# Optimization experiments

Measured on AMD Instinct MI355X. Metric: run time of the kernel, lower is better.

The kernel has to match this reference:

```python
import jax, jax.numpy as jnp
import numpy as np

B, D, H, W, C = 2, 28, 28, 28, 96
HEADS = 3
WS = (7, 7, 7)
SS = (3, 3, 3)
N = WS[0] * WS[1] * WS[2]  # 343 tokens per window
MLP_DIM = 4 * C


def _rel_pos_index():
    coords = np.stack(np.meshgrid(np.arange(WS[0]), np.arange(WS[1]), np.arange(WS[2]), indexing='ij'))
    cf = coords.reshape(3, -1)
    rel = (cf[:, :, None] - cf[:, None, :]).transpose(1, 2, 0)
    rel[..., 0] += WS[0] - 1
    rel[..., 1] += WS[1] - 1
    rel[..., 2] += WS[2] - 1
    rel[..., 0] *= (2 * WS[1] - 1) * (2 * WS[2] - 1)
    rel[..., 1] *= 2 * WS[2] - 1
    return rel.sum(-1)  # [N, N] int


def _compute_mask():
    # shifted-window attention mask (MONAI compute_mask)
    img = np.zeros((1, D, H, W, 1), np.float32)
    cnt = 0.0
    for ds in (slice(0, -WS[0]), slice(-WS[0], -SS[0]), slice(-SS[0], None)):
        for hs in (slice(0, -WS[1]), slice(-WS[1], -SS[1]), slice(-SS[1], None)):
            for ws_ in (slice(0, -WS[2]), slice(-WS[2], -SS[2]), slice(-SS[2], None)):
                img[:, ds, hs, ws_, :] = cnt
                cnt += 1.0
    mw = img.reshape(1, D // WS[0], WS[0], H // WS[1], WS[1], W // WS[2], WS[2], 1)
    mw = mw.transpose(0, 1, 3, 5, 2, 4, 6, 7).reshape(-1, N)  # [nw, N]
    diff = mw[:, None, :] - mw[:, :, None]
    return np.where(diff != 0, -100.0, 0.0).astype(np.float32)  # [nw, N, N]


def _ln(x, g, b):
    mu = x.mean(-1, keepdims=True)
    var = ((x - mu) ** 2).mean(-1, keepdims=True)
    return (x - mu) * jax.lax.rsqrt(var + 1e-5) * g + b


def setup_inputs() -> dict:
    key = jax.random.key(0)
    ks = jax.random.split(key, 8)
    f = lambda k, shape: (jax.random.normal(k, shape) * 0.02).astype(jnp.float32)
    n_bias = (2 * WS[0] - 1) * (2 * WS[1] - 1) * (2 * WS[2] - 1)
    return {
        'x': jax.random.normal(ks[0], (B, D, H, W, C), jnp.float32),
        'mask_matrix': jnp.asarray(_compute_mask()),
        'g1': jnp.ones((C,), jnp.float32), 'b1': jnp.zeros((C,), jnp.float32),
        'w_qkv': f(ks[1], (3 * C, C)), 'b_qkv': jnp.zeros((3 * C,), jnp.float32),
        'bias_table': f(ks[2], (n_bias, HEADS)),
        'w_proj': f(ks[3], (C, C)), 'b_proj': jnp.zeros((C,), jnp.float32),
        'g2': jnp.ones((C,), jnp.float32), 'b2': jnp.zeros((C,), jnp.float32),
        'w_fc1': f(ks[4], (MLP_DIM, C)), 'b_fc1': jnp.zeros((MLP_DIM,), jnp.float32),
        'w_fc2': f(ks[5], (C, MLP_DIM)), 'b_fc2': jnp.zeros((C,), jnp.float32),
        'rel_index': jnp.asarray(_rel_pos_index(), dtype=jnp.int32),
    }


def reference(x, mask_matrix, g1, b1, w_qkv, b_qkv, bias_table, w_proj, b_proj,
              g2, b2, w_fc1, b_fc1, w_fc2, b_fc2, rel_index):
    shortcut = x
    h = _ln(x, g1, b1)
    # cyclic shift
    h = jnp.roll(h, (-SS[0], -SS[1], -SS[2]), axis=(1, 2, 3))
    # window partition -> [B_, N, C]
    win = h.reshape(B, D // WS[0], WS[0], H // WS[1], WS[1], W // WS[2], WS[2], C)
    win = win.transpose(0, 1, 3, 5, 2, 4, 6, 7).reshape(-1, N, C)
    Bw = win.shape[0]
    hd = C // HEADS
    qkv = (win @ w_qkv.T + b_qkv).reshape(Bw, N, 3, HEADS, hd).transpose(2, 0, 3, 1, 4)
    q, k, v = qkv[0] * (hd ** -0.5), qkv[1], qkv[2]
    attn = jnp.einsum('bhnd,bhmd->bhnm', q, k)  # [Bw, H, N, N]
    bias = bias_table[rel_index.reshape(-1)].reshape(N, N, HEADS).transpose(2, 0, 1)
    attn = attn + bias[None]
    nw = mask_matrix.shape[0]
    attn = attn.reshape(Bw // nw, nw, HEADS, N, N) + mask_matrix[None, :, None]
    attn = jax.nn.softmax(attn.reshape(Bw, HEADS, N, N), axis=-1)
    out = jnp.einsum('bhnm,bhmd->bhnd', attn, v).transpose(0, 2, 1, 3).reshape(Bw, N, C)
    out = out @ w_proj.T + b_proj
    # window reverse -> [B, D, H, W, C]
    out = out.reshape(B, D // WS[0], H // WS[1], W // WS[2], WS[0], WS[1], WS[2], C)
    out = out.transpose(0, 1, 4, 2, 5, 3, 6, 7).reshape(B, D, H, W, C)
    # reverse cyclic shift
    out = jnp.roll(out, SS, axis=(1, 2, 3))
    x = shortcut + out
    h2 = _ln(x, g2, b2)
    h2 = jax.nn.gelu(h2 @ w_fc1.T + b_fc1, approximate=False)
    return x + (h2 @ w_fc2.T + b_fc2)
```

## Files before the change

kernel.cpp:

```cpp
#include <hip/hip_runtime.h>
#include <hip/hip_bf16.h>
#include <math.h>

typedef unsigned short u16;
typedef unsigned int u32;
typedef unsigned char u8;

#define T_TOK 43904
#define NTOK 343
#define LOG2E 1.4426950408889634f
#define MASKV 144.26950408889634f

typedef __attribute__((ext_vector_type(4))) float f32x4;
typedef __attribute__((ext_vector_type(8))) short s16x8;

__device__ __forceinline__ float bf2f(u32 v) { return __uint_as_float(v << 16); }
__device__ __forceinline__ u16 f2bf(float f) {
  u32 u = __float_as_uint(f);
  return (u16)((u + 0x7fffu + ((u >> 16) & 1u)) >> 16);
}

__device__ __forceinline__ float ldf(const void* p, int f32, size_t i) {
  return f32 ? ((const float*)p)[i] : bf2f(((const u16*)p)[i]);
}
__device__ __forceinline__ float2 ld2(const void* p, int f32, size_t i) {
  if (f32) return *(const float2*)((const float*)p + i);
  u32 pk = *(const u32*)((const u16*)p + i);
  return make_float2(bf2f(pk & 0xffff), bf2f(pk >> 16));
}

__device__ __forceinline__ size_t spatial_base(int t) {
  int win = t / 343, n = t - win * 343;
  int bb = win >> 6, wrem = win & 63;
  int wd = wrem >> 4, wh = (wrem >> 2) & 3, ww = wrem & 3;
  int td = n / 49; int r = n - td * 49; int th = r / 7; int tw = r - th * 7;
  int d0 = wd * 7 + td + 3; if (d0 >= 28) d0 -= 28;
  int h0 = wh * 7 + th + 3; if (h0 >= 28) h0 -= 28;
  int w0 = ww * 7 + tw + 3; if (w0 >= 28) w0 -= 28;
  return (size_t)(((bb * 28 + d0) * 28 + h0) * 28 + w0) * 96;
}

__device__ __forceinline__ int zone3(int p) { return p < 21 ? 0 : (p < 25 ? 1 : 2); }
__device__ __forceinline__ int cid_of(int mw, int n) {
  int td = n / 49, rr = n - td * 49, th = rr / 7, tw = rr - th * 7;
  int d = (mw >> 4) * 7 + td, h = ((mw >> 2) & 3) * 7 + th, w = (mw & 3) * 7 + tw;
  return zone3(d) * 9 + zone3(h) * 3 + zone3(w);
}

__global__ __launch_bounds__(64) void detect_kernel(const u16* __restrict__ x, int* __restrict__ flag) {
  int lane = threadIdx.x;
  int bad = 0;
  #pragma unroll
  for (int q = 0; q < 8; q++) {
    u16 b = x[(lane * 8 + q) * 2];
    int e = (b >> 7) & 0xff;
    if (e >= 0x90) bad = 1;
  }
  unsigned long long m = __ballot(bad);
  if (lane == 0) *flag = (m != 0ull) ? 1 : 0;
}

__global__ __launch_bounds__(256) void wconv_kernel(
    const void* __restrict__ w0, const void* __restrict__ w1,
    const void* __restrict__ w2, const void* __restrict__ w3,
    u16* __restrict__ out, const int* __restrict__ dflag) {
  int f32 = __builtin_amdgcn_readfirstlane(dflag[0]);
  int g = blockIdx.x * 256 + threadIdx.x;
  if (g >= 110592) return;
  float v;
  if (g < 27648)      v = ldf(w0, f32, g);
  else if (g < 36864) v = ldf(w1, f32, g - 27648);
  else if (g < 73728) v = ldf(w2, f32, g - 36864);
  else                v = ldf(w3, f32, g - 73728);
  out[g] = f2bf(v);
}

__global__ __launch_bounds__(256) void ln_gather_kernel(
    const void* __restrict__ x, const void* __restrict__ g, const void* __restrict__ b,
    u16* __restrict__ outw, const int* __restrict__ dflag) {
  int f32 = __builtin_amdgcn_readfirstlane(dflag[0]);
  int t = blockIdx.x * 4 + (threadIdx.x >> 6);
  int lane = threadIdx.x & 63;
  size_t base = spatial_base(t);
  int c = lane * 2;
  float vx = 0.f, vy = 0.f;
  if (c < 96) { float2 p = ld2(x, f32, base + c); vx = p.x; vy = p.y; }
  float s = vx + vy, ss = vx * vx + vy * vy;
  #pragma unroll
  for (int o = 1; o < 64; o <<= 1) { s += __shfl_xor(s, o); ss += __shfl_xor(ss, o); }
  float mean = s * (1.f / 96.f);
  float var = ss * (1.f / 96.f) - mean * mean;
  float rstd = rsqrtf(var + 1e-5f);
  if (c < 96) {
    float2 gp = ld2(g, f32, c), bp = ld2(b, f32, c);
    float y0 = (vx - mean) * rstd * gp.x + bp.x;
    float y1 = (vy - mean) * rstd * gp.y + bp.y;
    *(u32*)(outw + (size_t)t * 96 + c) = (u32)f2bf(y0) | ((u32)f2bf(y1) << 16);
  }
}

__global__ __launch_bounds__(256) void b3m_kernel(
    const void* __restrict__ bias_table, const int* __restrict__ rel,
    u16* __restrict__ b3m, const int* __restrict__ dflag) {
  int f32 = __builtin_amdgcn_readfirstlane(dflag[0]);
  int row = blockIdx.x;
  int by = blockIdx.y;
  int cls = by / 3, head = by - cls * 3;
  int mw = ((cls & 4) ? 48 : 0) | ((cls & 2) ? 12 : 0) | ((cls & 1) ? 3 : 0);
  int cidq = cid_of(mw, row);
  for (int col = threadIdx.x; col < 352; col += 256) {
    float v = -MASKV;
    if (col < 343) {
      v = ldf(bias_table, f32, (size_t)rel[row * 343 + col] * 3 + head) * LOG2E;
      if (cid_of(mw, col) != cidq) v -= MASKV;
    }
    b3m[((size_t)by * 343 + row) * 352 + col] = f2bf(v);
  }
}

__global__ __launch_bounds__(256) void qkv_kernel(
    const u16* __restrict__ A, const u16* __restrict__ Wb, const void* __restrict__ bias,
    u16* __restrict__ outp, const int* __restrict__ dflag) {
  int f32 = __builtin_amdgcn_readfirstlane(dflag[0]);
  __shared__ alignas(16) u16 As[128 * 104];
  __shared__ alignas(16) u16 Ws[96 * 104];
  int tid = threadIdx.x;
  int m0 = blockIdx.x * 128, n0 = blockIdx.y * 96;
  int w = tid >> 6, lane = tid & 63, quad = lane >> 4, l16 = lane & 15;
  f32x4 acc[2][6];
  #pragma unroll
  for (int i = 0; i < 2; i++)
    #pragma unroll
    for (int j = 0; j < 6; j++) acc[i][j] = (f32x4){0.f, 0.f, 0.f, 0.f};
  for (int i = tid; i < 1536; i += 256) {
    int row = i / 12; int c = (i - row * 12) * 8;
    *(uint4*)&As[row * 104 + c] = *(const uint4*)(A + (size_t)(m0 + row) * 96 + c);
  }
  for (int i = tid; i < 1152; i += 256) {
    int row = i / 12; int c = (i - row * 12) * 8;
    *(uint4*)&Ws[row * 104 + c] = *(const uint4*)(Wb + (size_t)(n0 + row) * 96 + c);
  }
  __syncthreads();
  #pragma unroll
  for (int kc = 0; kc < 3; kc++) {
    s16x8 fa0 = *(const s16x8*)&As[(w * 32 + l16) * 104 + kc * 32 + quad * 8];
    s16x8 fa1 = *(const s16x8*)&As[(w * 32 + 16 + l16) * 104 + kc * 32 + quad * 8];
    #pragma unroll
    for (int j = 0; j < 6; j++) {
      s16x8 fb = *(const s16x8*)&Ws[(j * 16 + l16) * 104 + kc * 32 + quad * 8];
      acc[0][j] = __builtin_amdgcn_mfma_f32_16x16x32_bf16(fa0, fb, acc[0][j], 0, 0, 0);
      acc[1][j] = __builtin_amdgcn_mfma_f32_16x16x32_bf16(fa1, fb, acc[1][j], 0, 0, 0);
    }
  }
  #pragma unroll
  for (int i = 0; i < 2; i++) {
    #pragma unroll
    for (int r = 0; r < 4; r++) {
      int mm = m0 + w * 32 + i * 16 + quad * 4 + r;
      #pragma unroll
      for (int j = 0; j < 6; j++) {
        int nn = n0 + j * 16 + l16;
        float v = acc[i][j][r] + ldf(bias, f32, nn);
        int sel = nn / 96, hd = (nn - sel * 96) >> 5, cc = nn & 31;
        float scl = (sel == 0) ? 0.25504208f : 1.0f;
        outp[((size_t)(sel * 3 + hd) * T_TOK + mm) * 32 + cc] = f2bf(v * scl);
      }
    }
  }
}

__device__ __forceinline__ int vsw(int ch) { return ((ch >> 1) ^ (ch >> 3)) & 3; }

__global__ __launch_bounds__(512) void attn_mfma_kernel(
    const u16* __restrict__ qkv, const u16* __restrict__ b3m,
    u16* __restrict__ attnb) {
  __shared__ alignas(16) u16 Ks[352 * 32];
  __shared__ alignas(16) u16 Vt[32 * 352];
  __shared__ alignas(16) u16 Ps[8][512];

  int tid = threadIdx.x;
  int wh = blockIdx.y;
  int head = wh % 3;
  int win = wh / 3;
  int mw = win & 63;
  int cls = (((mw >> 4) == 3) ? 4 : 0) | ((((mw >> 2) & 3) == 3) ? 2 : 0) | (((mw & 3) == 3) ? 1 : 0);
  int m0 = blockIdx.x * 128;
  size_t wbase = (size_t)win * NTOK;

  const u16* qplane = qkv + ((size_t)head * T_TOK + wbase) * 32;
  const u16* kplane = qkv + ((size_t)(3 + head) * T_TOK + wbase) * 32;
  const u16* vplane = qkv + ((size_t)(6 + head) * T_TOK + wbase) * 32;

  for (int i = tid; i < 1408; i += 512) {
    int tok = i >> 2, cb = i & 3;
    uint4 kv = make_uint4(0, 0, 0, 0);
    if (tok < 343) kv = *(const uint4*)(kplane + (size_t)tok * 32 + cb * 8);
    *(uint4*)&Ks[tok * 32 + 8 * (cb ^ (tok & 3))] = kv;
  }
  for (int i = tid; i < 688; i += 512) {
    int p = i >> 2, cb = (i & 3) * 8;
    int t0 = 2 * p;
    uint4 v0 = *(const uint4*)(vplane + (size_t)t0 * 32 + cb);
    uint4 v1 = make_uint4(0, 0, 0, 0);
    if (t0 + 1 < 343) v1 = *(const uint4*)(vplane + (size_t)(t0 + 1) * 32 + cb);
    u32 a0[4] = {v0.x, v0.y, v0.z, v0.w};
    u32 a1[4] = {v1.x, v1.y, v1.z, v1.w};
    int blk = t0 >> 3, tin = (t0 & 7) >> 1;
    #pragma unroll
    for (int q = 0; q < 4; q++) {
      int ch0 = cb + 2 * q;
      u32 w0v = (a0[q] & 0xffffu) | ((a1[q] & 0xffffu) << 16);
      u32 w1v = (a0[q] >> 16) | (a1[q] & 0xffff0000u);
      ((u32*)Vt)[ch0 * 176 + 4 * (blk ^ vsw(ch0)) + tin] = w0v;
      ((u32*)Vt)[(ch0 + 1) * 176 + 4 * (blk ^ vsw(ch0 + 1)) + tin] = w1v;
    }
  }
  if (tid < 256) {
    int ch = tid >> 3, j = tid & 7;
    Vt[ch * 352 + 8 * (43 ^ vsw(ch)) + j] = 0;
  }
  __syncthreads();

  int w = tid >> 6, lane = tid & 63, quad = lane >> 4, l16 = lane & 15;
  int qbase = m0 + w * 16;
  int qrow_l = qbase + l16;
  int qc = qrow_l < NTOK ? qrow_l : NTOK - 1;
  s16x8 fq = *(const s16x8*)(qplane + (size_t)qc * 32 + quad * 8);
  const u16* bmrow = b3m + ((size_t)(cls * 3 + head) * 343 + qc) * 352;
  int swl = (l16 ^ (l16 >> 2)) & 3;
  int vsw0 = vsw(l16), vsw1 = vsw(16 + l16);

  float lsum = 0.f;
  f32x4 o0 = {0.f, 0.f, 0.f, 0.f}, o1 = {0.f, 0.f, 0.f, 0.f};
  const f32x4 zz = {0.f, 0.f, 0.f, 0.f};

  for (int t32 = 0; t32 < 11; t32++) {
    #pragma unroll
    for (int h = 0; h < 2; h++) {
      int kb = t32 * 32 + h * 16;
      int ktok = kb + l16;
      s16x8 fk = *(const s16x8*)&Ks[ktok * 32 + 8 * (quad ^ (ktok & 3))];
      f32x4 st = __builtin_amdgcn_mfma_f32_16x16x32_bf16(fk, fq, zz, 0, 0, 0);
      uint2 bm = *(const uint2*)(bmrow + kb + quad * 4);
      float p0 = exp2f(st[0] + bf2f(bm.x & 0xffff));
      float p1 = exp2f(st[1] + bf2f(bm.x >> 16));
      float p2 = exp2f(st[2] + bf2f(bm.y & 0xffff));
      float p3 = exp2f(st[3] + bf2f(bm.y >> 16));
      lsum += (p0 + p1) + (p2 + p3);
      u32 pa = (__float_as_uint(p0) >> 16) | (__float_as_uint(p1) & 0xffff0000u);
      u32 pb = (__float_as_uint(p2) >> 16) | (__float_as_uint(p3) & 0xffff0000u);
      int blkp = h * 2 + (quad >> 1);
      *(uint2*)&Ps[w][l16 * 32 + 8 * (blkp ^ swl) + (quad & 1) * 4] = make_uint2(pa, pb);
    }
    s16x8 fp  = *(const s16x8*)&Ps[w][l16 * 32 + 8 * (quad ^ swl)];
    s16x8 fv0 = *(const s16x8*)&Vt[l16 * 352 + 8 * ((t32 * 4 + quad) ^ vsw0)];
    s16x8 fv1 = *(const s16x8*)&Vt[(16 + l16) * 352 + 8 * ((t32 * 4 + quad) ^ vsw1)];
    o0 = __builtin_amdgcn_mfma_f32_16x16x32_bf16(fp, fv0, o0, 0, 0, 0);
    o1 = __builtin_amdgcn_mfma_f32_16x16x32_bf16(fp, fv1, o1, 0, 0, 0);
  }

  lsum += __shfl_xor(lsum, 16);
  lsum += __shfl_xor(lsum, 32);
  #pragma unroll
  for (int r = 0; r < 4; r++) {
    int qrow = qbase + quad * 4 + r;
    float ls = __shfl(lsum, quad * 4 + r);
    if (qrow < NTOK) {
      float rs = 1.0f / ls;
      size_t ob = (wbase + qrow) * 96 + head * 32;
      attnb[ob + l16] = f2bf(o0[r] * rs);
      attnb[ob + 16 + l16] = f2bf(o1[r] * rs);
    }
  }
}

__global__ __launch_bounds__(256) void mlp_fused_kernel(
    const u16* __restrict__ attnb, const u16* __restrict__ wcat,
    const void* __restrict__ x, const void* __restrict__ b_proj,
    const void* __restrict__ g2, const void* __restrict__ b2,
    const void* __restrict__ b_fc1, const void* __restrict__ b_fc2,
    void* __restrict__ outp, const int* __restrict__ dflag) {
  int f32 = __builtin_amdgcn_readfirstlane(dflag[0]);
  __shared__ alignas(16) u16 As[64 * 104];
  __shared__ alignas(16) u16 As2[64 * 104];
  __shared__ alignas(16) u16 Ws[96 * 104];
  const u16* w_projb = wcat + 27648;
  const u16* w_fc1b  = wcat + 36864;
  const u16* w_fc2b  = wcat + 73728;
  int tid = threadIdx.x, m0 = blockIdx.x * 64;
  int w = tid >> 6, lane = tid & 63, quad = lane >> 4, l16 = lane & 15;

  for (int i = tid; i < 768; i += 256) {
    int row = i / 12, c = (i - row * 12) * 8;
    *(uint4*)&As[row * 104 + c] = *(const uint4*)(attnb + (size_t)(m0 + row) * 96 + c);
  }
  for (int i = tid; i < 1152; i += 256) {
    int row = i / 12, c = (i - row * 12) * 8;
    *(uint4*)&Ws[row * 104 + c] = *(const uint4*)(w_projb + row * 96 + c);
  }
  __syncthreads();
  f32x4 accp[6];
  #pragma unroll
  for (int j = 0; j < 6; j++) accp[j] = (f32x4){0.f, 0.f, 0.f, 0.f};
  #pragma unroll
  for (int kc = 0; kc < 3; kc++) {
    s16x8 fa = *(const s16x8*)&As[(w * 16 + l16) * 104 + kc * 32 + quad * 8];
    #pragma unroll
    for (int j = 0; j < 6; j++) {
      s16x8 fb = *(const s16x8*)&Ws[(j * 16 + l16) * 104 + kc * 32 + quad * 8];
      accp[j] = __builtin_amdgcn_mfma_f32_16x16x32_bf16(fa, fb, accp[j], 0, 0, 0);
    }
  }
  __syncthreads();

  float bp[6], gv[6], b2v[6];
  #pragma unroll
  for (int j = 0; j < 6; j++) {
    int nn = j * 16 + l16;
    bp[j] = ldf(b_proj, f32, nn); gv[j] = ldf(g2, f32, nn); b2v[j] = ldf(b2, f32, nn);
  }
  float rv[4][6];
  size_t sb[4];
  #pragma unroll
  for (int r = 0; r < 4; r++) {
    int mm = m0 + w * 16 + quad * 4 + r;
    sb[r] = spatial_base(mm);
    float s = 0.f, ss = 0.f;
    #pragma unroll
    for (int j = 0; j < 6; j++) {
      float v = accp[j][r] + bp[j] + ldf(x, f32, sb[r] + j * 16 + l16);
      rv[r][j] = v; s += v; ss += v * v;
    }
    #pragma unroll
    for (int o = 1; o < 16; o <<= 1) { s += __shfl_xor(s, o); ss += __shfl_xor(ss, o); }
    float mean = s * (1.f / 96.f);
    float var = ss * (1.f / 96.f) - mean * mean;
    float rstd = rsqrtf(var + 1e-5f);
    #pragma unroll
    for (int j = 0; j < 6; j++)
      As[(w * 16 + quad * 4 + r) * 104 + j * 16 + l16] = f2bf((rv[r][j] - mean) * rstd * gv[j] + b2v[j]);
  }

  f32x4 acc2[6];
  #pragma unroll
  for (int j = 0; j < 6; j++) acc2[j] = (f32x4){0.f, 0.f, 0.f, 0.f};
  for (int c = 0; c < 4; c++) {
    __syncthreads();
    for (int i = tid; i < 1152; i += 256) {
      int row = i / 12, cc = (i - row * 12) * 8;
      *(uint4*)&Ws[row * 104 + cc] = *(const uint4*)(w_fc1b + (size_t)(96 * c + row) * 96 + cc);
    }
    __syncthreads();
    f32x4 a1[6];
    #pragma unroll
    for (int j = 0; j < 6; j++) a1[j] = (f32x4){0.f, 0.f, 0.f, 0.f};
    #pragma unroll
    for (int kc = 0; kc < 3; kc++) {
      s16x8 fa = *(const s16x8*)&As[(w * 16 + l16) * 104 + kc * 32 + quad * 8];
      #pragma unroll
      for (int j = 0; j < 6; j++) {
        s16x8 fb = *(const s16x8*)&Ws[(j * 16 + l16) * 104 + kc * 32 + quad * 8];
        a1[j] = __builtin_amdgcn_mfma_f32_16x16x32_bf16(fa, fb, a1[j], 0, 0, 0);
      }
    }
    #pragma unroll
    for (int j = 0; j < 6; j++) {
      float bf1 = ldf(b_fc1, f32, 96 * c + j * 16 + l16);
      #pragma unroll
      for (int r = 0; r < 4; r++) {
        float v = a1[j][r] + bf1;
        v = 0.5f * v * (1.0f + erff(v * 0.70710678118f));
        As2[(w * 16 + quad * 4 + r) * 104 + j * 16 + l16] = f2bf(v);
      }
    }
    __syncthreads();
    for (int i = tid; i < 1152; i += 256) {
      int row = i / 12, cc = (i - row * 12) * 8;
      *(uint4*)&Ws[row * 104 + cc] = *(const uint4*)(w_fc2b + (size_t)row * 384 + 96 * c + cc);
    }
    __syncthreads();
    #pragma unroll
    for (int kc = 0; kc < 3; kc++) {
      s16x8 fa2 = *(const s16x8*)&As2[(w * 16 + l16) * 104 + kc * 32 + quad * 8];
      #pragma unroll
      for (int j = 0; j < 6; j++) {
        s16x8 fb = *(const s16x8*)&Ws[(j * 16 + l16) * 104 + kc * 32 + quad * 8];
        acc2[j] = __builtin_amdgcn_mfma_f32_16x16x32_bf16(fa2, fb, acc2[j], 0, 0, 0);
      }
    }
  }
  float bf2v[6];
  #pragma unroll
  for (int j = 0; j < 6; j++) bf2v[j] = ldf(b_fc2, f32, j * 16 + l16);
  #pragma unroll
  for (int r = 0; r < 4; r++) {
    #pragma unroll
    for (int j = 0; j < 6; j++) {
      float v = acc2[j][r] + bf2v[j] + rv[r][j];
      if (f32) ((float*)outp)[sb[r] + j * 16 + l16] = v;
      else     ((u16*)outp)[sb[r] + j * 16 + l16] = f2bf(v);
    }
  }
}

extern "C" void kernel_launch(void* const* d_in, const int* in_sizes, int n_in,
                              void* d_out, int out_size, void* d_ws, size_t ws_size,
                              hipStream_t stream) {
  (void)in_sizes; (void)n_in; (void)out_size; (void)ws_size;
  const void* x       = d_in[0];
  const void* g1      = d_in[2];
  const void* b1      = d_in[3];
  const void* w_qkv   = d_in[4];
  const void* b_qkv   = d_in[5];
  const void* bias_tb = d_in[6];
  const void* w_proj  = d_in[7];
  const void* b_proj  = d_in[8];
  const void* g2      = d_in[9];
  const void* b2      = d_in[10];
  const void* w_fc1   = d_in[11];
  const void* b_fc1   = d_in[12];
  const void* w_fc2   = d_in[13];
  const void* b_fc2   = d_in[14];
  const int* rel_idx  = (const int*)d_in[15];

  char* ws = (char*)d_ws;
  int*  dflag = (int*)ws;
  u16*  winb  = (u16*)(ws + 256);
  u16*  qkvb  = (u16*)(ws + 8429824);
  u16*  attnb = (u16*)(ws + 33718528);
  u16*  b3mb  = (u16*)(ws + 42148096);
  u16*  wcat  = (u16*)(ws + 47943424);
  u16*  w_qkvb = wcat;

  detect_kernel<<<1, 64, 0, stream>>>((const u16*)x, dflag);
  wconv_kernel<<<432, 256, 0, stream>>>(w_qkv, w_proj, w_fc1, w_fc2, wcat, dflag);
  b3m_kernel<<<dim3(343, 24), 256, 0, stream>>>(bias_tb, rel_idx, b3mb, dflag);
  ln_gather_kernel<<<T_TOK / 4, 256, 0, stream>>>(x, g1, b1, winb, dflag);
  qkv_kernel<<<dim3(343, 3), 256, 0, stream>>>(winb, w_qkvb, b_qkv, qkvb, dflag);
  attn_mfma_kernel<<<dim3(3, 384), 512, 0, stream>>>(qkvb, b3mb, attnb);
  mlp_fused_kernel<<<686, 256, 0, stream>>>(attnb, wcat, x, b_proj, g2, b2,
                                            b_fc1, b_fc2, d_out, dflag);
}
```

Before: 228.7 us.

## Fuse LN into QKV GEMM, merge setup kernels, prefetch MLP weights

```diff
diff --git a/kernel.cpp b/kernel.cpp
--- a/kernel.cpp
+++ b/kernel.cpp
@@ -23,10 +23,29 @@
 __device__ __forceinline__ float ldf(const void* p, int f32, size_t i) {
   return f32 ? ((const float*)p)[i] : bf2f(((const u16*)p)[i]);
 }
-__device__ __forceinline__ float2 ld2(const void* p, int f32, size_t i) {
-  if (f32) return *(const float2*)((const float*)p + i);
-  u32 pk = *(const u32*)((const u16*)p + i);
-  return make_float2(bf2f(pk & 0xffff), bf2f(pk >> 16));
+__device__ __forceinline__ void ld8(const void* p, int f32, size_t i, float* o) {
+  if (f32) {
+    float4 a = *(const float4*)((const float*)p + i);
+    float4 b = *(const float4*)((const float*)p + i + 4);
+    o[0] = a.x; o[1] = a.y; o[2] = a.z; o[3] = a.w;
+    o[4] = b.x; o[5] = b.y; o[6] = b.z; o[7] = b.w;
+  } else {
+    uint4 pk = *(const uint4*)((const u16*)p + i);
+    u32 v[4] = {pk.x, pk.y, pk.z, pk.w};
+    #pragma unroll
+    for (int q = 0; q < 4; q++) { o[2 * q] = bf2f(v[q] & 0xffff); o[2 * q + 1] = bf2f(v[q] >> 16); }
+  }
+}
+
+__device__ __forceinline__ int detect_f32x(const u16* xr) {
+  int lane = threadIdx.x & 63;
+  int bad = 0;
+  #pragma unroll
+  for (int q = 0; q < 8; q++) {
+    u16 b = xr[(lane * 8 + q) * 2];
+    if (((b >> 7) & 0xff) >= 0x90) bad = 1;
+  }
+  return (__ballot(bad) != 0ull) ? 1 : 0;
 }
 
 __device__ __forceinline__ size_t spatial_base(int t) {
@@ -47,100 +66,104 @@
   return zone3(d) * 9 + zone3(h) * 3 + zone3(w);
 }
 
-__global__ __launch_bounds__(64) void detect_kernel(const u16* __restrict__ x, int* __restrict__ flag) {
-  int lane = threadIdx.x;
-  int bad = 0;
-  #pragma unroll
-  for (int q = 0; q < 8; q++) {
-    u16 b = x[(lane * 8 + q) * 2];
-    int e = (b >> 7) & 0xff;
-    if (e >= 0x90) bad = 1;
-  }
-  unsigned long long m = __ballot(bad);
-  if (lane == 0) *flag = (m != 0ull) ? 1 : 0;
-}
-
-__global__ __launch_bounds__(256) void wconv_kernel(
+__global__ __launch_bounds__(256) void setup_kernel(
+    const u16* __restrict__ x,
     const void* __restrict__ w0, const void* __restrict__ w1,
     const void* __restrict__ w2, const void* __restrict__ w3,
-    u16* __restrict__ out, const int* __restrict__ dflag) {
-  int f32 = __builtin_amdgcn_readfirstlane(dflag[0]);
-  int g = blockIdx.x * 256 + threadIdx.x;
-  if (g >= 110592) return;
-  float v;
-  if (g < 27648)      v = ldf(w0, f32, g);
-  else if (g < 36864) v = ldf(w1, f32, g - 27648);
-  else if (g < 73728) v = ldf(w2, f32, g - 36864);
-  else                v = ldf(w3, f32, g - 73728);
-  out[g] = f2bf(v);
-}
-
-__global__ __launch_bounds__(256) void ln_gather_kernel(
-    const void* __restrict__ x, const void* __restrict__ g, const void* __restrict__ b,
-    u16* __restrict__ outw, const int* __restrict__ dflag) {
-  int f32 = __builtin_amdgcn_readfirstlane(dflag[0]);
-  int t = blockIdx.x * 4 + (threadIdx.x >> 6);
-  int lane = threadIdx.x & 63;
-  size_t base = spatial_base(t);
-  int c = lane * 2;
-  float vx = 0.f, vy = 0.f;
-  if (c < 96) { float2 p = ld2(x, f32, base + c); vx = p.x; vy = p.y; }
-  float s = vx + vy, ss = vx * vx + vy * vy;
-  #pragma unroll
-  for (int o = 1; o < 64; o <<= 1) { s += __shfl_xor(s, o); ss += __shfl_xor(ss, o); }
-  float mean = s * (1.f / 96.f);
-  float var = ss * (1.f / 96.f) - mean * mean;
-  float rstd = rsqrtf(var + 1e-5f);
-  if (c < 96) {
-    float2 gp = ld2(g, f32, c), bp = ld2(b, f32, c);
-    float y0 = (vx - mean) * rstd * gp.x + bp.x;
-    float y1 = (vy - mean) * rstd * gp.y + bp.y;
-    *(u32*)(outw + (size_t)t * 96 + c) = (u32)f2bf(y0) | ((u32)f2bf(y1) << 16);
-  }
-}
-
-__global__ __launch_bounds__(256) void b3m_kernel(
     const void* __restrict__ bias_table, const int* __restrict__ rel,
-    u16* __restrict__ b3m, const int* __restrict__ dflag) {
-  int f32 = __builtin_amdgcn_readfirstlane(dflag[0]);
-  int row = blockIdx.x;
-  int by = blockIdx.y;
-  int cls = by / 3, head = by - cls * 3;
-  int mw = ((cls & 4) ? 48 : 0) | ((cls & 2) ? 12 : 0) | ((cls & 1) ? 3 : 0);
-  int cidq = cid_of(mw, row);
-  for (int col = threadIdx.x; col < 352; col += 256) {
-    float v = -MASKV;
-    if (col < 343) {
-      v = ldf(bias_table, f32, (size_t)rel[row * 343 + col] * 3 + head) * LOG2E;
-      if (cid_of(mw, col) != cidq) v -= MASKV;
-    }
-    b3m[((size_t)by * 343 + row) * 352 + col] = f2bf(v);
-  }
-}
-
-__global__ __launch_bounds__(256) void qkv_kernel(
-    const u16* __restrict__ A, const u16* __restrict__ Wb, const void* __restrict__ bias,
-    u16* __restrict__ outp, const int* __restrict__ dflag) {
-  int f32 = __builtin_amdgcn_readfirstlane(dflag[0]);
+    u16* __restrict__ wcat, u16* __restrict__ b3m) {
+  int f32 = detect_f32x(x);
+  int b = blockIdx.x;
+  if (b < 432) {
+    int g = b * 256 + threadIdx.x;
+    if (g < 110592) {
+      float v;
+      if (g < 27648)      v = ldf(w0, f32, g);
+      else if (g < 36864) v = ldf(w1, f32, g - 27648);
+      else if (g < 73728) v = ldf(w2, f32, g - 36864);
+      else                v = ldf(w3, f32, g - 73728);
+      wcat[g] = f2bf(v);
+    }
+    return;
+  }
+  int row = b - 432;
+  for (int by = 0; by < 24; by++) {
+    int cls = by / 3, head = by - cls * 3;
+    int mw = ((cls & 4) ? 48 : 0) | ((cls & 2) ? 12 : 0) | ((cls & 1) ? 3 : 0);
+    int cidq = cid_of(mw, row);
+    for (int col = threadIdx.x; col < 352; col += 256) {
+      float v = -MASKV;
+      if (col < 343) {
+        v = ldf(bias_table, f32, (size_t)rel[row * 343 + col] * 3 + head) * LOG2E;
+        if (cid_of(mw, col) != cidq) v -= MASKV;
+      }
+      b3m[((size_t)by * 343 + row) * 352 + col] = f2bf(v);
+    }
+  }
+}
+
+__global__ __launch_bounds__(256) void qkv_ln_kernel(
+    const void* __restrict__ x, const void* __restrict__ g1, const void* __restrict__ b1,
+    const u16* __restrict__ Wb, const void* __restrict__ bias,
+    u16* __restrict__ outp) {
+  int f32 = detect_f32x((const u16*)x);
   __shared__ alignas(16) u16 As[128 * 104];
   __shared__ alignas(16) u16 Ws[96 * 104];
+  __shared__ float gld[96], bld[96];
   int tid = threadIdx.x;
   int m0 = blockIdx.x * 128, n0 = blockIdx.y * 96;
   int w = tid >> 6, lane = tid & 63, quad = lane >> 4, l16 = lane & 15;
+
+  for (int i = tid; i < 1536; i += 256) {
+    int row = i / 12, cc = (i - row * 12) * 8;
+    size_t sb = spatial_base(m0 + row);
+    float f[8];
+    ld8(x, f32, sb + cc, f);
+    uint4 pk;
+    pk.x = (u32)f2bf(f[0]) | ((u32)f2bf(f[1]) << 16);
+    pk.y = (u32)f2bf(f[2]) | ((u32)f2bf(f[3]) << 16);
+    pk.z = (u32)f2bf(f[4]) | ((u32)f2bf(f[5]) << 16);
+    pk.w = (u32)f2bf(f[6]) | ((u32)f2bf(f[7]) << 16);
+    *(uint4*)&As[row * 104 + cc] = pk;
+  }
+  for (int i = tid; i < 1152; i += 256) {
+    int row = i / 12, cc = (i - row * 12) * 8;
+    *(uint4*)&Ws[row * 104 + cc] = *(const uint4*)(Wb + (size_t)(n0 + row) * 96 + cc);
+  }
+  if (tid < 96) { gld[tid] = ldf(g1, f32, tid); bld[tid] = ldf(b1, f32, tid); }
+  __syncthreads();
+
+  {
+    int row = tid >> 1, half = tid & 1;
+    u32* rp = (u32*)&As[row * 104] + half * 24;
+    float s = 0.f, ss = 0.f;
+    #pragma unroll
+    for (int m = 0; m < 24; m++) {
+      u32 pk = rp[m];
+      float a = bf2f(pk & 0xffff), b = bf2f(pk >> 16);
+      s += a + b; ss += a * a + b * b;
+    }
+    s += __shfl_xor(s, 1); ss += __shfl_xor(ss, 1);
+    float mean = s * (1.f / 96.f);
+    float var = ss * (1.f / 96.f) - mean * mean;
+    float rstd = rsqrtf(var + 1e-5f);
+    int cbase = half * 48;
+    #pragma unroll
+    for (int m = 0; m < 24; m++) {
+      u32 pk = rp[m];
+      float a = bf2f(pk & 0xffff), b = bf2f(pk >> 16);
+      a = (a - mean) * rstd * gld[cbase + 2 * m] + bld[cbase + 2 * m];
+      b = (b - mean) * rstd * gld[cbase + 2 * m + 1] + bld[cbase + 2 * m + 1];
+      rp[m] = (u32)f2bf(a) | ((u32)f2bf(b) << 16);
+    }
+  }
+  __syncthreads();
+
   f32x4 acc[2][6];
   #pragma unroll
   for (int i = 0; i < 2; i++)
     #pragma unroll
     for (int j = 0; j < 6; j++) acc[i][j] = (f32x4){0.f, 0.f, 0.f, 0.f};
-  for (int i = tid; i < 1536; i += 256) {
-    int row = i / 12; int c = (i - row * 12) * 8;
-    *(uint4*)&As[row * 104 + c] = *(const uint4*)(A + (size_t)(m0 + row) * 96 + c);
-  }
-  for (int i = tid; i < 1152; i += 256) {
-    int row = i / 12; int c = (i - row * 12) * 8;
-    *(uint4*)&Ws[row * 104 + c] = *(const uint4*)(Wb + (size_t)(n0 + row) * 96 + c);
-  }
-  __syncthreads();
   #pragma unroll
   for (int kc = 0; kc < 3; kc++) {
     s16x8 fa0 = *(const s16x8*)&As[(w * 32 + l16) * 104 + kc * 32 + quad * 8];
@@ -274,13 +297,35 @@
   }
 }
 
+struct PF { uint4 v[5]; };
+__device__ __forceinline__ void pf_load(PF& p, const u16* base, int rowstride, int coloff, int tid) {
+  #pragma unroll
+  for (int t = 0; t < 5; t++) {
+    int idx = tid + t * 256;
+    if (idx < 1152) {
+      int row = idx / 12, cc = (idx - row * 12) * 8;
+      p.v[t] = *(const uint4*)(base + (size_t)row * rowstride + coloff + cc);
+    }
+  }
+}
+__device__ __forceinline__ void pf_commit(const PF& p, u16* Ws, int tid) {
+  #pragma unroll
+  for (int t = 0; t < 5; t++) {
+    int idx = tid + t * 256;
+    if (idx < 1152) {
+      int row = idx / 12, cc = (idx - row * 12) * 8;
+      *(uint4*)&Ws[row * 104 + cc] = p.v[t];
+    }
+  }
+}
+
 __global__ __launch_bounds__(256) void mlp_fused_kernel(
     const u16* __restrict__ attnb, const u16* __restrict__ wcat,
     const void* __restrict__ x, const void* __restrict__ b_proj,
     const void* __restrict__ g2, const void* __restrict__ b2,
     const void* __restrict__ b_fc1, const void* __restrict__ b_fc2,
-    void* __restrict__ outp, const int* __restrict__ dflag) {
-  int f32 = __builtin_amdgcn_readfirstlane(dflag[0]);
+    void* __restrict__ outp) {
+  int f32 = detect_f32x((const u16*)x);
   __shared__ alignas(16) u16 As[64 * 104];
   __shared__ alignas(16) u16 As2[64 * 104];
   __shared__ alignas(16) u16 Ws[96 * 104];
@@ -290,15 +335,17 @@
   int tid = threadIdx.x, m0 = blockIdx.x * 64;
   int w = tid >> 6, lane = tid & 63, quad = lane >> 4, l16 = lane & 15;
 
+  PF p;
+  pf_load(p, w_projb, 96, 0, tid);
   for (int i = tid; i < 768; i += 256) {
     int row = i / 12, c = (i - row * 12) * 8;
     *(uint4*)&As[row * 104 + c] = *(const uint4*)(attnb + (size_t)(m0 + row) * 96 + c);
   }
-  for (int i = tid; i < 1152; i += 256) {
-    int row = i / 12, c = (i - row * 12) * 8;
-    *(uint4*)&Ws[row * 104 + c] = *(const uint4*)(w_projb + row * 96 + c);
-  }
   __syncthreads();
+  pf_commit(p, Ws, tid);
+  pf_load(p, w_fc1b, 96, 0, tid);
+  __syncthreads();
+
   f32x4 accp[6];
   #pragma unroll
   for (int j = 0; j < 6; j++) accp[j] = (f32x4){0.f, 0.f, 0.f, 0.f};
@@ -311,7 +358,6 @@
       accp[j] = __builtin_amdgcn_mfma_f32_16x16x32_bf16(fa, fb, accp[j], 0, 0, 0);
     }
   }
-  __syncthreads();
 
   float bp[6], gv[6], b2v[6];
   #pragma unroll
@@ -346,10 +392,8 @@
   for (int j = 0; j < 6; j++) acc2[j] = (f32x4){0.f, 0.f, 0.f, 0.f};
   for (int c = 0; c < 4; c++) {
     __syncthreads();
-    for (int i = tid; i < 1152; i += 256) {
-      int row = i / 12, cc = (i - row * 12) * 8;
-      *(uint4*)&Ws[row * 104 + cc] = *(const uint4*)(w_fc1b + (size_t)(96 * c + row) * 96 + cc);
-    }
+    pf_commit(p, Ws, tid);
+    pf_load(p, w_fc2b, 384, 96 * c, tid);
     __syncthreads();
     f32x4 a1[6];
     #pragma unroll
@@ -374,10 +418,8 @@
       }
     }
     __syncthreads();
-    for (int i = tid; i < 1152; i += 256) {
-      int row = i / 12, cc = (i - row * 12) * 8;
-      *(uint4*)&Ws[row * 104 + cc] = *(const uint4*)(w_fc2b + (size_t)row * 384 + 96 * c + cc);
-    }
+    pf_commit(p, Ws, tid);
+    if (c < 3) pf_load(p, w_fc1b + (size_t)96 * (c + 1) * 96, 96, 0, tid);
     __syncthreads();
     #pragma unroll
     for (int kc = 0; kc < 3; kc++) {
@@ -424,20 +466,16 @@
   const int* rel_idx  = (const int*)d_in[15];
 
   char* ws = (char*)d_ws;
-  int*  dflag = (int*)ws;
-  u16*  winb  = (u16*)(ws + 256);
-  u16*  qkvb  = (u16*)(ws + 8429824);
-  u16*  attnb = (u16*)(ws + 33718528);
-  u16*  b3mb  = (u16*)(ws + 42148096);
-  u16*  wcat  = (u16*)(ws + 47943424);
+  u16*  qkvb  = (u16*)(ws + 256);
+  u16*  attnb = (u16*)(ws + 256 + 25288704);
+  u16*  b3mb  = (u16*)(ws + 256 + 25288704 + 8429568);
+  u16*  wcat  = (u16*)(ws + 256 + 25288704 + 8429568 + 5795328);
   u16*  w_qkvb = wcat;
 
-  detect_kernel<<<1, 64, 0, stream>>>((const u16*)x, dflag);
-  wconv_kernel<<<432, 256, 0, stream>>>(w_qkv, w_proj, w_fc1, w_fc2, wcat, dflag);
-  b3m_kernel<<<dim3(343, 24), 256, 0, stream>>>(bias_tb, rel_idx, b3mb, dflag);
-  ln_gather_kernel<<<T_TOK / 4, 256, 0, stream>>>(x, g1, b1, winb, dflag);
-  qkv_kernel<<<dim3(343, 3), 256, 0, stream>>>(winb, w_qkvb, b_qkv, qkvb, dflag);
+  setup_kernel<<<775, 256, 0, stream>>>((const u16*)x, w_qkv, w_proj, w_fc1, w_fc2,
+                                        bias_tb, rel_idx, wcat, b3mb);
+  qkv_ln_kernel<<<dim3(343, 3), 256, 0, stream>>>(x, g1, b1, w_qkvb, b_qkv, qkvb);
   attn_mfma_kernel<<<dim3(3, 384), 512, 0, stream>>>(qkvb, b3mb, attnb);
   mlp_fused_kernel<<<686, 256, 0, stream>>>(attnb, wcat, x, b_proj, g2, b2,
-                                            b_fc1, b_fc2, d_out, dflag);
-}
+                                            b_fc1, b_fc2, d_out);
+}
```

Result: slower. 293.4 us (+28.3%).
